# Performance work log

Measured on AMD Instinct MI355X. Metric: run time of the kernel, lower is better.

The kernel has to match this reference:

```python
import jax, jax.numpy as jnp
import numpy as np

# shift search range (matches init_kwargs)
MIN_SX, MAX_SX = -4, 4
MIN_SY, MAX_SY = -4, 4
B, C, H, W = 4, 3, 512, 512


def _shift(x, sx, sy):
    """torch.roll on dims (1,2) of a [C,H,W] tensor, zeroing wrapped rows/cols.

    Equivalent to AutomatedShiftFix.shift: positive sx zeros rows [:sx],
    negative sx zeros rows [sx:]; same for sy on the W axis.
    """
    h, w = x.shape[1], x.shape[2]
    shifted = jnp.roll(x, (sx, sy), axis=(1, 2))
    i = jnp.arange(h)[:, None]   # [H,1]
    j = jnp.arange(w)[None, :]   # [1,W]
    mask_h = jnp.where(sx >= 0, i >= sx, i < h + sx)
    mask_w = jnp.where(sy >= 0, j >= sy, j < w + sy)
    mask = (mask_h & mask_w).astype(x.dtype)  # [H,W]
    return shifted * mask[None]


def _all_shifts():
    sx = jnp.arange(MIN_SX, MAX_SX + 1)
    sy = jnp.arange(MIN_SY, MAX_SY + 1)
    # outer loop over shift_x, inner over shift_y -> 'ij' matches torch ordering
    return jnp.stack(jnp.meshgrid(sx, sy, indexing="ij"), axis=-1).reshape(-1, 2)  # [Ns,2]


def setup_inputs() -> dict:
    key = jax.random.key(0)
    k1, k2 = jax.random.split(key)
    x_ref = jax.random.normal(k1, (B, C, H, W), dtype=jnp.float32)
    x = jax.random.normal(k2, (B, C, H, W), dtype=jnp.float32)
    return {"x_ref": x_ref, "x": x}


def reference(x_ref, x):
    shifts = _all_shifts()  # [Ns,2] int32

    def sims_one(xr, xi):  # xr, xi: [C,H,W]
        # similarity for every candidate shift: sum over (C,H,W) of shifted*ref
        return jax.vmap(lambda s: jnp.sum(_shift(xi, s[0], s[1]) * xr))(shifts)  # [Ns]

    sims = jax.vmap(sims_one)(x_ref, x)          # [B, Ns]
    best = jnp.argmax(sims, axis=1)              # [B]
    best_shifts = shifts[best]                   # [B, 2]
    out = jax.vmap(lambda xi, s: _shift(xi, s[0], s[1]))(x, best_shifts)  # [B,C,H,W]
    return out, best_shifts
```

## Files before the change

kernel.cpp:

```cpp
#include <hip/hip_runtime.h>

#define BB 4
#define CC 3
#define HH 512
#define WW 512
#define NS 81
#define IMG (HH * WW)
#define CHW (CC * IMG)
#define STRIP 8
#define NSTRIPS (HH / STRIP)
#define NBLK (BB * CC * NSTRIPS)
#define SLOTS (CC * NSTRIPS)

__device__ double g_part[(size_t)BB * NS * SLOTS];
__device__ int    g_best[BB];

#define C4(v, i) ((i) == 0 ? (v).x : (i) == 1 ? (v).y : (i) == 2 ? (v).z : (v).w)

__global__ __launch_bounds__(576, 4) void k_sims(const float* __restrict__ xref,
                                                 const float* __restrict__ x) {
    int raw   = blockIdx.x;
    int bid   = (raw & 7) * (NBLK / 8) + (raw >> 3);
    int strip = bid % NSTRIPS;
    int bc    = bid / NSTRIPS;
    int b     = bc / CC;
    const float* xp = x    + (size_t)bc * IMG;
    const float* rp = xref + (size_t)bc * IMG;
    int tid  = threadIdx.x;
    int lane = tid & 63;
    int sxi  = tid >> 6;
    int j0   = lane << 3;
    int sx   = sxi - 4;
    int ip0  = strip * STRIP;

    float acc[9];
#pragma unroll
    for (int s = 0; s < 9; ++s) acc[s] = 0.f;

#pragma unroll
    for (int rr = 0; rr < STRIP; ++rr) {
        int ip = ip0 + rr;
        int ii = ip + sx;
        if ((unsigned)ii >= HH) continue;

        const float* xrow = xp + ip * WW + j0;
        const float* rrow = rp + ii * WW + j0;
        float4 xa = *(const float4*)(xrow);
        float4 xb = *(const float4*)(xrow + 4);

        const float4* pp = (const float4*)(rrow + (lane == 0  ? 0 : -4));
        const float4* np = (const float4*)(rrow + (lane == 63 ? 0 :  8));
        float4 pv = *pp;
        float4 ra = *(const float4*)(rrow);
        float4 rb = *(const float4*)(rrow + 4);
        float4 nv = *np;
        if (lane == 0)  pv = make_float4(0.f, 0.f, 0.f, 0.f);
        if (lane == 63) nv = make_float4(0.f, 0.f, 0.f, 0.f);

#pragma unroll
        for (int syi = 0; syi < 9; ++syi) {
#pragma unroll
            for (int k = 0; k < 8; ++k) {
                int i = k + syi;
                float wv = (i < 4)  ? C4(pv, i)
                         : (i < 8)  ? C4(ra, i - 4)
                         : (i < 12) ? C4(rb, i - 8)
                         :            C4(nv, i - 12);
                float xv = (k < 4) ? C4(xa, k) : C4(xb, k - 4);
                acc[syi] += xv * wv;
            }
        }
    }

    int cs = (bc % CC) * NSTRIPS + strip;
#pragma unroll
    for (int s = 0; s < 9; ++s) {
        float v = acc[s];
        for (int off = 32; off; off >>= 1) v += __shfl_down(v, off, 64);
        if (lane == 0)
            g_part[((size_t)b * NS + sxi * 9 + s) * SLOTS + cs] = (double)v;
    }
}

__global__ __launch_bounds__(128) void k_reduce(float* __restrict__ outTail) {
    int b = blockIdx.x;
    int t = threadIdx.x;
    __shared__ double vals[NS];
    if (t < NS) {
        const double* p = g_part + ((size_t)b * NS + t) * SLOTS;
        double s0 = 0.0, s1 = 0.0;
        for (int i = 0; i < SLOTS; i += 2) { s0 += p[i]; s1 += p[i + 1]; }
        vals[t] = s0 + s1;
    }
    __syncthreads();
    if (t == 0) {
        int best = 0;
        double bv = vals[0];
        for (int i = 1; i < NS; ++i)
            if (vals[i] > bv) { bv = vals[i]; best = i; }
        g_best[b] = best;
        outTail[b * 2]     = (float)(best / 9 - 4);
        outTail[b * 2 + 1] = (float)(best % 9 - 4);
    }
}

__global__ __launch_bounds__(256) void k_apply(const float* __restrict__ x,
                                               float* __restrict__ out) {
    int blk = blockIdx.x;
    int bc  = blk >> 8;
    int tid = threadIdx.x;
    int b   = bc / CC;

    int bi = g_best[b];
    int sx = bi / 9 - 4;
    int sy = bi % 9 - 4;

    int row = ((blk & 255) << 1) + (tid >> 7);
    int j0  = (tid & 127) << 2;
    int is  = row - sx;
    float4 v = make_float4(0.f, 0.f, 0.f, 0.f);
    if ((unsigned)is < HH) {
        const float* src = x + (size_t)bc * IMG + is * WW;
        int js0 = j0 - sy;
        if (js0 >= 0 && js0 + 3 < WW) {
            v = *(const float4*)(src + js0);
        } else {
            float* vv = (float*)&v;
#pragma unroll
            for (int k = 0; k < 4; ++k) {
                int js = js0 + k;
                if ((unsigned)js < WW) vv[k] = src[js];
            }
        }
    }
    *(float4*)(out + (size_t)bc * IMG + row * WW + j0) = v;
}

extern "C" void kernel_launch(void* const* d_in, const int* in_sizes, int n_in,
                              void* d_out, int out_size, void* d_ws, size_t ws_size,
                              hipStream_t stream) {
    const float* xref = (const float*)d_in[0];
    const float* x    = (const float*)d_in[1];
    float* out = (float*)d_out;
    (void)d_ws; (void)ws_size;

    k_sims<<<NBLK, 576, 0, stream>>>(xref, x);
    k_reduce<<<BB, 128, 0, stream>>>(out + (size_t)BB * CHW);

    int applyBlocks = (BB * CC * HH) / 2;
    k_apply<<<applyBlocks, 256, 0, stream>>>(x, out);
}
```

Before: 101.7 us.

## Stage x and reference strip rows in swizzled LDS for reuse across shifts

Each block now loads its 8-row strip of x and the 16 reference rows it needs into shared memory once, using an XOR swizzle on float4 columns, then reads all per-shift operands from LDS. Before, each wave issued its own global loads for overlapping reference rows. The block-index remapping across XCDs is also removed. In exchange the kernel uses about 48KB of LDS per block, which may cap occupancy at one block per CU, and it adds a barrier.

New measurement: 101.8 us. About the same (+0.0%).

```diff
diff --git a/kernel.cpp b/kernel.cpp
--- a/kernel.cpp
+++ b/kernel.cpp
@@ -17,10 +17,14 @@
 
 #define C4(v, i) ((i) == 0 ? (v).x : (i) == 1 ? (v).y : (i) == 2 ? (v).z : (v).w)
 
+__device__ __forceinline__ int swz(int c) { return (c ^ ((c >> 3) & 7)) << 2; }
+
 __global__ __launch_bounds__(576, 4) void k_sims(const float* __restrict__ xref,
                                                  const float* __restrict__ x) {
-    int raw   = blockIdx.x;
-    int bid   = (raw & 7) * (NBLK / 8) + (raw >> 3);
+    __shared__ float xS[STRIP * WW];
+    __shared__ float refS[(STRIP + 8) * WW];
+
+    int bid   = blockIdx.x;
     int strip = bid % NSTRIPS;
     int bc    = bid / NSTRIPS;
     int b     = bc / CC;
@@ -29,9 +33,38 @@
     int tid  = threadIdx.x;
     int lane = tid & 63;
     int sxi  = tid >> 6;
-    int j0   = lane << 3;
     int sx   = sxi - 4;
     int ip0  = strip * STRIP;
+
+    for (int t = sxi; t < 2 * (STRIP + 16); t += 9) {
+        int half = t & 1;
+        int r    = t >> 1;
+        const float* gsrc;
+        float* lbase;
+        bool ok = true;
+        if (r < STRIP) {
+            gsrc  = xp + (size_t)(ip0 + r) * WW;
+            lbase = xS + r * WW;
+        } else {
+            int rl = r - STRIP;
+            int gr = ip0 - 4 + rl;
+            ok    = (unsigned)gr < HH;
+            gsrc  = rp + (size_t)gr * WW;
+            lbase = refS + rl * WW;
+        }
+        if (ok) {
+            int c = half * 64 + lane;
+            float4 v = *(const float4*)(gsrc + c * 4);
+            *(float4*)(lbase + swz(c)) = v;
+        }
+    }
+    __syncthreads();
+
+    int c0  = lane * 2;
+    int pc0 = swz(c0);
+    int pc1 = swz(c0 + 1);
+    int pcm = swz(lane == 0  ? 0   : c0 - 1);
+    int pcp = swz(lane == 63 ? 127 : c0 + 2);
 
     float acc[9];
 #pragma unroll
@@ -39,21 +72,17 @@
 
 #pragma unroll
     for (int rr = 0; rr < STRIP; ++rr) {
-        int ip = ip0 + rr;
-        int ii = ip + sx;
+        int ii = ip0 + rr + sx;
         if ((unsigned)ii >= HH) continue;
 
-        const float* xrow = xp + ip * WW + j0;
-        const float* rrow = rp + ii * WW + j0;
-        float4 xa = *(const float4*)(xrow);
-        float4 xb = *(const float4*)(xrow + 4);
-
-        const float4* pp = (const float4*)(rrow + (lane == 0  ? 0 : -4));
-        const float4* np = (const float4*)(rrow + (lane == 63 ? 0 :  8));
-        float4 pv = *pp;
-        float4 ra = *(const float4*)(rrow);
-        float4 rb = *(const float4*)(rrow + 4);
-        float4 nv = *np;
+        const float* xrow = xS   + rr * WW;
+        const float* rrow = refS + (rr + sx + 4) * WW;
+        float4 xa = *(const float4*)(xrow + pc0);
+        float4 xb = *(const float4*)(xrow + pc1);
+        float4 ra = *(const float4*)(rrow + pc0);
+        float4 rb = *(const float4*)(rrow + pc1);
+        float4 pv = *(const float4*)(rrow + pcm);
+        float4 nv = *(const float4*)(rrow + pcp);
         if (lane == 0)  pv = make_float4(0.f, 0.f, 0.f, 0.f);
         if (lane == 63) nv = make_float4(0.f, 0.f, 0.f, 0.f);
 
```
